# Kernel optimization log

Hardware: AMD Instinct MI355X
Metric: run time of the kernel (lower is better)

Reference implementation:

```python
import jax, jax.numpy as jnp
import numpy as np

S = 1.0   # scale s
M = 0.4   # margin m
EPS = 1e-12  # F.normalize eps


def _l2norm_rows(a):
    # F.normalize(a, dim=1): row-wise L2 normalization
    n = jnp.linalg.norm(a, axis=1, keepdims=True)
    return a / jnp.maximum(n, EPS)


def _half_loss(sim):
    # unique-label branch: positive is the diagonal, all off-diagonal are negatives
    N = sim.shape[0]
    num = S * (jnp.diagonal(sim) - M)                       # [N]
    offdiag = jnp.exp(S * sim) * (1.0 - jnp.eye(N, dtype=sim.dtype))
    denom = jnp.exp(num) + jnp.sum(offdiag, axis=1)         # [N]
    return num - jnp.log(denom)


def setup_inputs() -> dict:
    key = jax.random.key(0)
    k1, k2 = jax.random.split(key)
    N, D = 8192, 256
    return {
        "x1": jax.random.normal(k1, (N, D), dtype=jnp.float32),
        "x2": jax.random.normal(k2, (N, D), dtype=jnp.float32),
        "sentence_id": jnp.arange(N, dtype=jnp.int32),  # unique labels -> more_label=False branch
    }


def reference(x1, x2, sentence_id):
    # x12[i,j] row-normalized similarity of x1_i against all x2_j (and symmetric)
    x12 = _l2norm_rows(x1 @ x2.T)   # [N, N]
    x21 = _l2norm_rows(x2 @ x1.T)   # [N, N]
    L12 = _half_loss(x12)
    L21 = _half_loss(x21)
    loss = -jnp.mean(L12) - jnp.mean(L21)
    return loss, L12, L21
```

## Files before the change

kernel.cpp:

```cpp
#include <hip/hip_runtime.h>
#include <cstdint>
#include <cstddef>


#define NROWS 8192
#define DIMK 256
#define MARGIN 0.4f
#define LOG2E 1.4426950408889634f
#define LN2 0.6931471805599453f

typedef short short8 __attribute__((ext_vector_type(8)));
typedef float f32x4 __attribute__((ext_vector_type(4)));

__device__ __forceinline__ unsigned short f2bf(float f) {
  union { float f; unsigned u; } v; v.f = f;
  unsigned r = (v.u + 0x7fffu + ((v.u >> 16) & 1u)) >> 16;
  return (unsigned short)r;
}

__device__ __forceinline__ void gl_lds16(const void* g, void* l) {
  __builtin_amdgcn_global_load_lds((const __attribute__((address_space(1))) void*)g,
                                   (__attribute__((address_space(3))) void*)l, 16, 0, 0);
}

__device__ __forceinline__ float fexp(float x) {
  return __builtin_amdgcn_exp2f(x * LOG2E);
}

__global__ __launch_bounds__(256)
void k_prep(const float* __restrict__ x1, const float* __restrict__ x2,
            unsigned short* __restrict__ Ab, unsigned short* __restrict__ Bb,
            float* __restrict__ diag, float* __restrict__ zero_region) {
  const int t = threadIdx.x;
  if (blockIdx.x < 2048) {
    const int row = blockIdx.x * 4 + (t >> 6);
    const int l = t & 63;
    const float4 a = ((const float4*)(x1 + (size_t)row * DIMK))[l];
    const float4 b = ((const float4*)(x2 + (size_t)row * DIMK))[l];
    ushort4 ua, ub;
    ua.x = f2bf(a.x); ua.y = f2bf(a.y); ua.z = f2bf(a.z); ua.w = f2bf(a.w);
    ub.x = f2bf(b.x); ub.y = f2bf(b.y); ub.z = f2bf(b.z); ub.w = f2bf(b.w);
    ((ushort4*)(Ab + (size_t)row * DIMK))[l] = ua;
    ((ushort4*)(Bb + (size_t)row * DIMK))[l] = ub;
    float d = a.x * b.x + a.y * b.y + a.z * b.z + a.w * b.w;
#pragma unroll
    for (int m = 1; m < 64; m <<= 1) d += __shfl_xor(d, m);
    if (l == 0) diag[row] = d;
  } else {
    const size_t off = (size_t)(blockIdx.x - 2048) * 1024 + t * 4;
    float4 z = {0.f, 0.f, 0.f, 0.f};
    *(float4*)(zero_region + off) = z;
  }
}

__global__ __launch_bounds__(256)
void k_syrk(const unsigned short* __restrict__ Ab, const unsigned short* __restrict__ Bb,
            float* __restrict__ M1, float* __restrict__ M2) {
  __shared__ unsigned short As[64 * 32];
  __shared__ unsigned short Bs[64 * 32];
  const int t = threadIdx.x, w = t >> 6, l = t & 63, quad = l >> 4, l15 = l & 15;
  const int mat = blockIdx.z & 1;
  const int kseg = blockIdx.z >> 1;
  const unsigned short* X = mat ? Bb : Ab;
  float* Mo = mat ? M2 : M1;
  const int a0 = blockIdx.y * 64, b0 = blockIdx.x * 64;
  const int wr = (w >> 1) * 32, wc = (w & 1) * 32;
  f32x4 acc[2][2] = {};
  const int nn = t & 31, cb = t >> 5;
  const int c0 = cb * 8;
  const int nb = kseg * 512;
  for (int n0 = nb; n0 < nb + 512; n0 += 32) {
    short8 va = *(const short8*)(X + (size_t)(n0 + nn) * DIMK + a0 + c0);
    short8 vb = *(const short8*)(X + (size_t)(n0 + nn) * DIMK + b0 + c0);
#pragma unroll
    for (int i = 0; i < 8; ++i) {
      const int c = c0 + i;
      const int sl = (((nn >> 3) ^ ((c >> 1) & 3)) << 3) + (nn & 7);
      As[c * 32 + sl] = va[i];
      Bs[c * 32 + sl] = vb[i];
    }
    __syncthreads();
    short8 af[2], bg[2];
#pragma unroll
    for (int i = 0; i < 2; ++i) {
      const int ra = wr + i * 16 + l15;
      af[i] = *(const short8*)&As[ra * 32 + ((quad ^ ((ra >> 1) & 3)) << 3)];
      const int rb = wc + i * 16 + l15;
      bg[i] = *(const short8*)&Bs[rb * 32 + ((quad ^ ((rb >> 1) & 3)) << 3)];
    }
#pragma unroll
    for (int i = 0; i < 2; ++i)
#pragma unroll
      for (int j = 0; j < 2; ++j)
        acc[i][j] = __builtin_amdgcn_mfma_f32_16x16x32_bf16(af[i], bg[j], acc[i][j], 0, 0, 0);
    __syncthreads();
  }
#pragma unroll
  for (int i = 0; i < 2; ++i)
#pragma unroll
    for (int j = 0; j < 2; ++j)
#pragma unroll
      for (int r = 0; r < 4; ++r) {
        const int lr = wr + i * 16 + quad * 4 + r;
        const int lc = wc + j * 16 + l15;
        atomicAdd(&Mo[(size_t)(a0 + lr) * 256 + b0 + lc], acc[i][j][r]);
      }
}

__global__ __launch_bounds__(256)
void k_gemmN(const unsigned short* __restrict__ Ab, const unsigned short* __restrict__ Bb,
             const float* __restrict__ M1, const float* __restrict__ M2,
             const float* __restrict__ x1, const float* __restrict__ x2,
             float* __restrict__ rowsq, float* __restrict__ colsq) {
  __shared__ unsigned short As[2][4096];
  __shared__ unsigned short Bs[2][4096];
  const int t = threadIdx.x, w = t >> 6, l = t & 63, quad = l >> 4, l15 = l & 15;
  const unsigned short* A;
  const float* Mf;
  const float* Xf;
  float* sq;
  if (blockIdx.z == 0) { A = Ab; Mf = M2; Xf = x1; sq = rowsq; }
  else                 { A = Bb; Mf = M1; Xf = x2; sq = colsq; }
  const int row0 = blockIdx.x * 128;
  const int col0 = blockIdx.y * 128;
  const int wr = (w >> 1) * 64, wc = (w & 1) * 64;
  f32x4 acc[4][4] = {};

  const int sr0 = l >> 2, slot = l & 3;
  const int cA = w * 2, cB = w * 2 + 1;
  const int rA = cA * 16 + sr0, rB = cB * 16 + sr0;
  const int scA = (slot ^ ((rA >> 1) & 3)) << 3;
  const int scB = (slot ^ ((rB >> 1) & 3)) << 3;
  const unsigned short* pA0 = A + (size_t)(row0 + rA) * DIMK + scA;
  const unsigned short* pA1 = A + (size_t)(row0 + rB) * DIMK + scB;
  const int dA0 = cA * 512 + l * 8, dA1 = cB * 512 + l * 8;

  auto stageB = [&](int k0, int buf) {
#pragma unroll
    for (int g = 0; g < 2; ++g) {
      const int e = g * 2048 + t * 8;
      const int c = e >> 5, kk = e & 31;
      const float4 v0 = *(const float4*)(Mf + (size_t)(col0 + c) * 256 + k0 + kk);
      const float4 v1 = *(const float4*)(Mf + (size_t)(col0 + c) * 256 + k0 + kk + 4);
      ushort4 u0, u1;
      u0.x = f2bf(v0.x); u0.y = f2bf(v0.y); u0.z = f2bf(v0.z); u0.w = f2bf(v0.w);
      u1.x = f2bf(v1.x); u1.y = f2bf(v1.y); u1.z = f2bf(v1.z); u1.w = f2bf(v1.w);
      const int sw = ((kk >> 3) ^ ((c >> 1) & 3)) << 3;
      *(ushort4*)&Bs[buf][c * 32 + sw] = u0;
      *(ushort4*)&Bs[buf][c * 32 + sw + 4] = u1;
    }
  };
  auto issueA = [&](int k0, int buf) {
    gl_lds16(pA0 + k0, &As[buf][dA0]);
    gl_lds16(pA1 + k0, &As[buf][dA1]);
  };

  stageB(0, 0);
  issueA(0, 0);
#pragma unroll
  for (int k = 0; k < 8; ++k) {
    const int cur = k & 1;
    __syncthreads();
    if (k < 7) { stageB((k + 1) * 32, cur ^ 1); issueA((k + 1) * 32, cur ^ 1); }
    short8 af[4], bg[4];
#pragma unroll
    for (int i = 0; i < 4; ++i) {
      const int ra = wr + i * 16 + l15;
      af[i] = *(const short8*)&As[cur][ra * 32 + ((quad ^ ((ra >> 1) & 3)) << 3)];
      const int rb = wc + i * 16 + l15;
      bg[i] = *(const short8*)&Bs[cur][rb * 32 + ((quad ^ ((rb >> 1) & 3)) << 3)];
    }
#pragma unroll
    for (int i = 0; i < 4; ++i)
#pragma unroll
      for (int j = 0; j < 4; ++j)
        acc[i][j] = __builtin_amdgcn_mfma_f32_16x16x32_bf16(af[i], bg[j], acc[i][j], 0, 0, 0);
  }

#pragma unroll
  for (int i = 0; i < 4; ++i) {
#pragma unroll
    for (int r = 0; r < 4; ++r) {
      const int lr = wr + i * 16 + quad * 4 + r;
      const float* xr = Xf + (size_t)(row0 + lr) * DIMK + col0 + wc;
      float rp = 0.f;
#pragma unroll
      for (int j = 0; j < 4; ++j) rp += acc[i][j][r] * xr[j * 16 + l15];
      rp += __shfl_xor(rp, 1); rp += __shfl_xor(rp, 2);
      rp += __shfl_xor(rp, 4); rp += __shfl_xor(rp, 8);
      if (l15 == 0) atomicAdd(&sq[row0 + lr], rp);
    }
  }
}

__global__ __launch_bounds__(256)
void k_gemmE(const unsigned short* __restrict__ Abuf, const unsigned short* __restrict__ Bbuf,
             const float* __restrict__ rowsq, const float* __restrict__ colsq,
             float* __restrict__ rowExp, float* __restrict__ colExp) {
  __shared__ unsigned short As[2][4096];
  __shared__ unsigned short Bs[2][4096];
  __shared__ float cRow[128];
  __shared__ float cCol[128];

  const int t = threadIdx.x;
  const int w = t >> 6;
  const int l = t & 63;
  const int quad = l >> 4;
  const int l15 = l & 15;
  const int row0 = blockIdx.x * 128;
  const int col0 = blockIdx.y * 128;
  const int wr = (w >> 1) * 64;
  const int wc = (w & 1) * 64;

  if (t < 128) cRow[t] = LOG2E * rsqrtf(rowsq[row0 + t]);
  else cCol[t - 128] = LOG2E * rsqrtf(colsq[col0 + t - 128]);

  f32x4 acc[4][4] = {};

  const int sr0 = l >> 2;
  const int slot = l & 3;
  const int cA = w * 2, cB = w * 2 + 1;
  const int rA = cA * 16 + sr0, rB = cB * 16 + sr0;
  const int scA = (slot ^ ((rA >> 1) & 3)) << 3;
  const int scB = (slot ^ ((rB >> 1) & 3)) << 3;
  const unsigned short* pA0 = Abuf + (size_t)(row0 + rA) * DIMK + scA;
  const unsigned short* pA1 = Abuf + (size_t)(row0 + rB) * DIMK + scB;
  const unsigned short* pB0 = Bbuf + (size_t)(col0 + rA) * DIMK + scA;
  const unsigned short* pB1 = Bbuf + (size_t)(col0 + rB) * DIMK + scB;
  const int dA0 = cA * 512 + l * 8, dA1 = cB * 512 + l * 8;

  gl_lds16(pA0, &As[0][dA0]);
  gl_lds16(pA1, &As[0][dA1]);
  gl_lds16(pB0, &Bs[0][dA0]);
  gl_lds16(pB1, &Bs[0][dA1]);

#pragma unroll
  for (int k0 = 0; k0 < 8; ++k0) {
    const int cur = k0 & 1;
    __syncthreads();
    if (k0 < 7) {
      const int nxt = cur ^ 1;
      gl_lds16(pA0 + (k0 + 1) * 32, &As[nxt][dA0]);
      gl_lds16(pA1 + (k0 + 1) * 32, &As[nxt][dA1]);
      gl_lds16(pB0 + (k0 + 1) * 32, &Bs[nxt][dA0]);
      gl_lds16(pB1 + (k0 + 1) * 32, &Bs[nxt][dA1]);
    }
    short8 af[4], bg[4];
#pragma unroll
    for (int i = 0; i < 4; ++i) {
      const int ra = wr + i * 16 + l15;
      af[i] = *(const short8*)&As[cur][ra * 32 + ((quad ^ ((ra >> 1) & 3)) << 3)];
      const int rb = wc + i * 16 + l15;
      bg[i] = *(const short8*)&Bs[cur][rb * 32 + ((quad ^ ((rb >> 1) & 3)) << 3)];
    }
#pragma unroll
    for (int i = 0; i < 4; ++i)
#pragma unroll
      for (int j = 0; j < 4; ++j)
        acc[i][j] = __builtin_amdgcn_mfma_f32_16x16x32_bf16(af[i], bg[j], acc[i][j], 0, 0, 0);
  }

  float cj[4];
#pragma unroll
  for (int j = 0; j < 4; ++j) cj[j] = cCol[wc + j * 16 + l15];
  float colpart[4] = {0.f, 0.f, 0.f, 0.f};
#pragma unroll
  for (int i = 0; i < 4; ++i) {
#pragma unroll
    for (int r = 0; r < 4; ++r) {
      const int lr = wr + i * 16 + quad * 4 + r;
      const float ci = cRow[lr];
      float rp = 0.f;
#pragma unroll
      for (int j = 0; j < 4; ++j) {
        const float g = acc[i][j][r];
        rp += __builtin_amdgcn_exp2f(g * ci);
        colpart[j] += __builtin_amdgcn_exp2f(g * cj[j]);
      }
      rp += __shfl_xor(rp, 1); rp += __shfl_xor(rp, 2);
      rp += __shfl_xor(rp, 4); rp += __shfl_xor(rp, 8);
      if (l15 == 0) atomicAdd(&rowExp[row0 + lr], rp);
    }
  }
#pragma unroll
  for (int j = 0; j < 4; ++j) {
    float cp = colpart[j];
    cp += __shfl_xor(cp, 16); cp += __shfl_xor(cp, 32);
    if (l < 16) atomicAdd(&colExp[col0 + wc + j * 16 + l15], cp);
  }
}

__global__ __launch_bounds__(1024)
void k_final(const float* __restrict__ rowsq, const float* __restrict__ colsq,
             const float* __restrict__ diag, const float* __restrict__ rowExp,
             const float* __restrict__ colExp, float* __restrict__ out,
             double* __restrict__ lossAcc, int* __restrict__ doneCnt) {
  const int t = threadIdx.x;
  const int i = blockIdx.x * 1024 + t;
  const float d = diag[i];
  const float s1 = d * rsqrtf(rowsq[i]);
  const float s2 = d * rsqrtf(colsq[i]);
  const float n1 = s1 - MARGIN, n2 = s2 - MARGIN;
  const float L1 = n1 - LN2 * __builtin_amdgcn_logf(rowExp[i] - fexp(s1) + fexp(n1));
  const float L2 = n2 - LN2 * __builtin_amdgcn_logf(colExp[i] - fexp(s2) + fexp(n2));
  out[1 + i] = L1;
  out[1 + NROWS + i] = L2;
  double part = (double)L1 + (double)L2;
#pragma unroll
  for (int m = 1; m < 64; m <<= 1) part += __shfl_xor(part, m);
  __shared__ double red[16];
  if ((t & 63) == 0) red[t >> 6] = part;
  __syncthreads();
  if (t == 0) {
    double s = 0.0;
#pragma unroll
    for (int q = 0; q < 16; ++q) s += red[q];
    atomicAdd(lossAcc, s);
    __threadfence();
    if (atomicAdd(doneCnt, 1) == 7) {
      const double la =
          __hip_atomic_load(lossAcc, __ATOMIC_ACQUIRE, __HIP_MEMORY_SCOPE_AGENT);
      out[0] = (float)(-la / (double)NROWS);
    }
  }
}

extern "C" void kernel_launch(void* const* d_in, const int* in_sizes, int n_in,
                              void* d_out, int out_size, void* d_ws, size_t ws_size,
                              hipStream_t stream) {
  const float* x1 = (const float*)d_in[0];
  const float* x2 = (const float*)d_in[1];
  float* out = (float*)d_out;
  char* ws = (char*)d_ws;

  unsigned short* Ab = (unsigned short*)(ws);
  unsigned short* Bb = (unsigned short*)(ws + 4194304);
  float* M1 = (float*)(ws + 8388608);
  float* M2 = (float*)(ws + 8650752);
  float* rowsq = (float*)(ws + 8912896);
  float* colsq = (float*)(ws + 8945664);
  float* rowExp = (float*)(ws + 8978432);
  float* colExp = (float*)(ws + 9011200);
  char* ctrl = ws + 9043968;
  double* lossAcc = (double*)(ctrl);
  int* doneCnt = (int*)(ctrl + 256);
  float* diag = (float*)(ws + 9048064);

  k_prep<<<2209, 256, 0, stream>>>(x1, x2, Ab, Bb, diag, (float*)(ws + 8388608));
  k_syrk<<<dim3(4, 4, 32), 256, 0, stream>>>(Ab, Bb, M1, M2);
  k_gemmN<<<dim3(64, 2, 2), 256, 0, stream>>>(Ab, Bb, M1, M2, x1, x2, rowsq, colsq);
  k_gemmE<<<dim3(64, 64), 256, 0, stream>>>(Ab, Bb, rowsq, colsq, rowExp, colExp);
  k_final<<<8, 1024, 0, stream>>>(rowsq, colsq, diag, rowExp, colExp, out,
                                  lossAcc, doneCnt);
}
```

Measured before the change: 191.5 us.

## Load GEMM operands directly to registers and remap blocks for XCD locality

The exp-GEMM kernel drops its LDS double buffering and barriers. Each wave now loads its MFMA fragments straight from global memory into registers, prefetching one k-step ahead. The grid is flattened and remapped so that blocks on the same XCD share column tiles, which is meant to improve L2 reuse. In exchange, each wave issues redundant global loads (operands are no longer shared through LDS), and the row/column scale factors are recomputed per thread instead of being staged in shared memory.

```diff
diff --git a/kernel.cpp b/kernel.cpp
--- a/kernel.cpp
+++ b/kernel.cpp
@@ -197,84 +197,71 @@
 void k_gemmE(const unsigned short* __restrict__ Abuf, const unsigned short* __restrict__ Bbuf,
              const float* __restrict__ rowsq, const float* __restrict__ colsq,
              float* __restrict__ rowExp, float* __restrict__ colExp) {
-  __shared__ unsigned short As[2][4096];
-  __shared__ unsigned short Bs[2][4096];
-  __shared__ float cRow[128];
-  __shared__ float cCol[128];
-
-  const int t = threadIdx.x;
-  const int w = t >> 6;
-  const int l = t & 63;
-  const int quad = l >> 4;
-  const int l15 = l & 15;
-  const int row0 = blockIdx.x * 128;
-  const int col0 = blockIdx.y * 128;
-  const int wr = (w >> 1) * 64;
-  const int wc = (w & 1) * 64;
-
-  if (t < 128) cRow[t] = LOG2E * rsqrtf(rowsq[row0 + t]);
-  else cCol[t - 128] = LOG2E * rsqrtf(colsq[col0 + t - 128]);
+  const int t = threadIdx.x, w = t >> 6, l = t & 63, quad = l >> 4, l15 = l & 15;
+  const int b = blockIdx.x;
+  const int xcd = b & 7, s = b >> 3;
+  const int col0 = (xcd * 8 + (s & 7)) * 128;
+  const int row0 = (s >> 3) * 128;
+  const int wr = (w >> 1) * 64, wc = (w & 1) * 64;
+
+  const unsigned short* pA[4];
+  const unsigned short* pB[4];
+#pragma unroll
+  for (int i = 0; i < 4; ++i) {
+    pA[i] = Abuf + (size_t)(row0 + wr + i * 16 + l15) * DIMK + quad * 8;
+    pB[i] = Bbuf + (size_t)(col0 + wc + i * 16 + l15) * DIMK + quad * 8;
+  }
 
   f32x4 acc[4][4] = {};
-
-  const int sr0 = l >> 2;
-  const int slot = l & 3;
-  const int cA = w * 2, cB = w * 2 + 1;
-  const int rA = cA * 16 + sr0, rB = cB * 16 + sr0;
-  const int scA = (slot ^ ((rA >> 1) & 3)) << 3;
-  const int scB = (slot ^ ((rB >> 1) & 3)) << 3;
-  const unsigned short* pA0 = Abuf + (size_t)(row0 + rA) * DIMK + scA;
-  const unsigned short* pA1 = Abuf + (size_t)(row0 + rB) * DIMK + scB;
-  const unsigned short* pB0 = Bbuf + (size_t)(col0 + rA) * DIMK + scA;
-  const unsigned short* pB1 = Bbuf + (size_t)(col0 + rB) * DIMK + scB;
-  const int dA0 = cA * 512 + l * 8, dA1 = cB * 512 + l * 8;
-
-  gl_lds16(pA0, &As[0][dA0]);
-  gl_lds16(pA1, &As[0][dA1]);
-  gl_lds16(pB0, &Bs[0][dA0]);
-  gl_lds16(pB1, &Bs[0][dA1]);
+  short8 a_cur[4], b_cur[4];
+#pragma unroll
+  for (int i = 0; i < 4; ++i) {
+    a_cur[i] = *(const short8*)pA[i];
+    b_cur[i] = *(const short8*)pB[i];
+  }
 
 #pragma unroll
   for (int k0 = 0; k0 < 8; ++k0) {
-    const int cur = k0 & 1;
-    __syncthreads();
+    short8 a_nxt[4], b_nxt[4];
     if (k0 < 7) {
-      const int nxt = cur ^ 1;
-      gl_lds16(pA0 + (k0 + 1) * 32, &As[nxt][dA0]);
-      gl_lds16(pA1 + (k0 + 1) * 32, &As[nxt][dA1]);
-      gl_lds16(pB0 + (k0 + 1) * 32, &Bs[nxt][dA0]);
-      gl_lds16(pB1 + (k0 + 1) * 32, &Bs[nxt][dA1]);
-    }
-    short8 af[4], bg[4];
-#pragma unroll
-    for (int i = 0; i < 4; ++i) {
-      const int ra = wr + i * 16 + l15;
-      af[i] = *(const short8*)&As[cur][ra * 32 + ((quad ^ ((ra >> 1) & 3)) << 3)];
-      const int rb = wc + i * 16 + l15;
-      bg[i] = *(const short8*)&Bs[cur][rb * 32 + ((quad ^ ((rb >> 1) & 3)) << 3)];
+#pragma unroll
+      for (int i = 0; i < 4; ++i) {
+        a_nxt[i] = *(const short8*)(pA[i] + (k0 + 1) * 32);
+        b_nxt[i] = *(const short8*)(pB[i] + (k0 + 1) * 32);
+      }
     }
 #pragma unroll
     for (int i = 0; i < 4; ++i)
 #pragma unroll
       for (int j = 0; j < 4; ++j)
-        acc[i][j] = __builtin_amdgcn_mfma_f32_16x16x32_bf16(af[i], bg[j], acc[i][j], 0, 0, 0);
+        acc[i][j] = __builtin_amdgcn_mfma_f32_16x16x32_bf16(a_cur[i], b_cur[j], acc[i][j], 0, 0, 0);
+    if (k0 < 7) {
+#pragma unroll
+      for (int i = 0; i < 4; ++i) { a_cur[i] = a_nxt[i]; b_cur[i] = b_nxt[i]; }
+    }
   }
 
   float cj[4];
 #pragma unroll
-  for (int j = 0; j < 4; ++j) cj[j] = cCol[wc + j * 16 + l15];
+  for (int j = 0; j < 4; ++j)
+    cj[j] = LOG2E * rsqrtf(colsq[col0 + wc + j * 16 + l15]);
+  float ci[4][4];
+#pragma unroll
+  for (int i = 0; i < 4; ++i)
+#pragma unroll
+    for (int r = 0; r < 4; ++r)
+      ci[i][r] = LOG2E * rsqrtf(rowsq[row0 + wr + i * 16 + quad * 4 + r]);
   float colpart[4] = {0.f, 0.f, 0.f, 0.f};
 #pragma unroll
   for (int i = 0; i < 4; ++i) {
 #pragma unroll
     for (int r = 0; r < 4; ++r) {
       const int lr = wr + i * 16 + quad * 4 + r;
-      const float ci = cRow[lr];
       float rp = 0.f;
 #pragma unroll
       for (int j = 0; j < 4; ++j) {
         const float g = acc[i][j][r];
-        rp += __builtin_amdgcn_exp2f(g * ci);
+        rp += __builtin_amdgcn_exp2f(g * ci[i][r]);
         colpart[j] += __builtin_amdgcn_exp2f(g * cj[j]);
       }
       rp += __shfl_xor(rp, 1); rp += __shfl_xor(rp, 2);
@@ -349,7 +336,7 @@
   k_prep<<<2209, 256, 0, stream>>>(x1, x2, Ab, Bb, diag, (float*)(ws + 8388608));
   k_syrk<<<dim3(4, 4, 32), 256, 0, stream>>>(Ab, Bb, M1, M2);
   k_gemmN<<<dim3(64, 2, 2), 256, 0, stream>>>(Ab, Bb, M1, M2, x1, x2, rowsq, colsq);
-  k_gemmE<<<dim3(64, 64), 256, 0, stream>>>(Ab, Bb, rowsq, colsq, rowExp, colExp);
+  k_gemmE<<<4096, 256, 0, stream>>>(Ab, Bb, rowsq, colsq, rowExp, colExp);
   k_final<<<8, 1024, 0, stream>>>(rowsq, colsq, diag, rowExp, colExp, out,
                                   lossAcc, doneCnt);
 }
```

New measurement: 282.2 us. +47.4%, slower.

## Widen gemmE tiles to 128x256 with XCD-aware mapping; split gemmN K

Applied to the files above, without the earlier changes.

The main exp-GEMM kernel now computes a 128x256 tile per block instead of 128x128, with each wave holding a 64x128 accumulator (32 MFMA tiles). This halves A-tile reloads and atomics per output element, and blocks are mapped to columns per XCD so B tiles stay in the local L2. gemmN gets a split-K over two halves of K, doubling its grid to raise parallelism, with partial results combined through the existing atomics. The cost is higher register pressure and more LDS per block in gemmE, which may reduce occupancy.

```diff
diff --git a/kernel.cpp b/kernel.cpp
--- a/kernel.cpp
+++ b/kernel.cpp
@@ -119,8 +119,9 @@
   const float* Mf;
   const float* Xf;
   float* sq;
-  if (blockIdx.z == 0) { A = Ab; Mf = M2; Xf = x1; sq = rowsq; }
-  else                 { A = Bb; Mf = M1; Xf = x2; sq = colsq; }
+  if ((blockIdx.z & 1) == 0) { A = Ab; Mf = M2; Xf = x1; sq = rowsq; }
+  else                       { A = Bb; Mf = M1; Xf = x2; sq = colsq; }
+  const int kbase = (blockIdx.z >> 1) * 128;
   const int row0 = blockIdx.x * 128;
   const int col0 = blockIdx.y * 128;
   const int wr = (w >> 1) * 64, wc = (w & 1) * 64;
@@ -131,8 +132,8 @@
   const int rA = cA * 16 + sr0, rB = cB * 16 + sr0;
   const int scA = (slot ^ ((rA >> 1) & 3)) << 3;
   const int scB = (slot ^ ((rB >> 1) & 3)) << 3;
-  const unsigned short* pA0 = A + (size_t)(row0 + rA) * DIMK + scA;
-  const unsigned short* pA1 = A + (size_t)(row0 + rB) * DIMK + scB;
+  const unsigned short* pA0 = A + (size_t)(row0 + rA) * DIMK + kbase + scA;
+  const unsigned short* pA1 = A + (size_t)(row0 + rB) * DIMK + kbase + scB;
   const int dA0 = cA * 512 + l * 8, dA1 = cB * 512 + l * 8;
 
   auto stageB = [&](int k0, int buf) {
@@ -140,8 +141,8 @@
     for (int g = 0; g < 2; ++g) {
       const int e = g * 2048 + t * 8;
       const int c = e >> 5, kk = e & 31;
-      const float4 v0 = *(const float4*)(Mf + (size_t)(col0 + c) * 256 + k0 + kk);
-      const float4 v1 = *(const float4*)(Mf + (size_t)(col0 + c) * 256 + k0 + kk + 4);
+      const float4 v0 = *(const float4*)(Mf + (size_t)(col0 + c) * 256 + kbase + k0 + kk);
+      const float4 v1 = *(const float4*)(Mf + (size_t)(col0 + c) * 256 + kbase + k0 + kk + 4);
       ushort4 u0, u1;
       u0.x = f2bf(v0.x); u0.y = f2bf(v0.y); u0.z = f2bf(v0.z); u0.w = f2bf(v0.w);
       u1.x = f2bf(v1.x); u1.y = f2bf(v1.y); u1.z = f2bf(v1.z); u1.w = f2bf(v1.w);
@@ -158,10 +159,10 @@
   stageB(0, 0);
   issueA(0, 0);
 #pragma unroll
-  for (int k = 0; k < 8; ++k) {
+  for (int k = 0; k < 4; ++k) {
     const int cur = k & 1;
     __syncthreads();
-    if (k < 7) { stageB((k + 1) * 32, cur ^ 1); issueA((k + 1) * 32, cur ^ 1); }
+    if (k < 3) { stageB((k + 1) * 32, cur ^ 1); issueA((k + 1) * 32, cur ^ 1); }
     short8 af[4], bg[4];
 #pragma unroll
     for (int i = 0; i < 4; ++i) {
@@ -198,72 +199,79 @@
              const float* __restrict__ rowsq, const float* __restrict__ colsq,
              float* __restrict__ rowExp, float* __restrict__ colExp) {
   __shared__ unsigned short As[2][4096];
-  __shared__ unsigned short Bs[2][4096];
+  __shared__ unsigned short Bs[2][8192];
   __shared__ float cRow[128];
-  __shared__ float cCol[128];
+  __shared__ float cCol[256];
 
   const int t = threadIdx.x;
   const int w = t >> 6;
   const int l = t & 63;
   const int quad = l >> 4;
   const int l15 = l & 15;
-  const int row0 = blockIdx.x * 128;
-  const int col0 = blockIdx.y * 128;
+  const int b = blockIdx.x;
+  const int xcd = b & 7, s = b >> 3;
+  const int col0 = (xcd * 4 + (s & 3)) * 256;
+  const int row0 = (s >> 2) * 128;
   const int wr = (w >> 1) * 64;
-  const int wc = (w & 1) * 64;
+  const int wc = (w & 1) * 128;
 
   if (t < 128) cRow[t] = LOG2E * rsqrtf(rowsq[row0 + t]);
-  else cCol[t - 128] = LOG2E * rsqrtf(colsq[col0 + t - 128]);
-
-  f32x4 acc[4][4] = {};
+  cCol[t] = LOG2E * rsqrtf(colsq[col0 + t]);
+
+  f32x4 acc[4][8] = {};
 
   const int sr0 = l >> 2;
   const int slot = l & 3;
-  const int cA = w * 2, cB = w * 2 + 1;
-  const int rA = cA * 16 + sr0, rB = cB * 16 + sr0;
-  const int scA = (slot ^ ((rA >> 1) & 3)) << 3;
-  const int scB = (slot ^ ((rB >> 1) & 3)) << 3;
-  const unsigned short* pA0 = Abuf + (size_t)(row0 + rA) * DIMK + scA;
-  const unsigned short* pA1 = Abuf + (size_t)(row0 + rB) * DIMK + scB;
-  const unsigned short* pB0 = Bbuf + (size_t)(col0 + rA) * DIMK + scA;
-  const unsigned short* pB1 = Bbuf + (size_t)(col0 + rB) * DIMK + scB;
-  const int dA0 = cA * 512 + l * 8, dA1 = cB * 512 + l * 8;
-
-  gl_lds16(pA0, &As[0][dA0]);
-  gl_lds16(pA1, &As[0][dA1]);
-  gl_lds16(pB0, &Bs[0][dA0]);
-  gl_lds16(pB1, &Bs[0][dA1]);
-
+  const int cA0 = w * 2, cA1 = w * 2 + 1;
+  const int rA0 = cA0 * 16 + sr0, rA1 = cA1 * 16 + sr0;
+  const unsigned short* pA0 = Abuf + (size_t)(row0 + rA0) * DIMK + ((slot ^ ((rA0 >> 1) & 3)) << 3);
+  const unsigned short* pA1 = Abuf + (size_t)(row0 + rA1) * DIMK + ((slot ^ ((rA1 >> 1) & 3)) << 3);
+  const int dA0 = cA0 * 512 + l * 8, dA1 = cA1 * 512 + l * 8;
+  const unsigned short* pB[4];
+  int dB[4];
+#pragma unroll
+  for (int p = 0; p < 4; ++p) {
+    const int c = w * 4 + p;
+    const int r = c * 16 + sr0;
+    pB[p] = Bbuf + (size_t)(col0 + r) * DIMK + ((slot ^ ((r >> 1) & 3)) << 3);
+    dB[p] = c * 512 + l * 8;
+  }
+
+  auto issue = [&](int k0, int buf) {
+    gl_lds16(pA0 + k0, &As[buf][dA0]);
+    gl_lds16(pA1 + k0, &As[buf][dA1]);
+#pragma unroll
+    for (int p = 0; p < 4; ++p) gl_lds16(pB[p] + k0, &Bs[buf][dB[p]]);
+  };
+
+  issue(0, 0);
 #pragma unroll
   for (int k0 = 0; k0 < 8; ++k0) {
     const int cur = k0 & 1;
     __syncthreads();
-    if (k0 < 7) {
-      const int nxt = cur ^ 1;
-      gl_lds16(pA0 + (k0 + 1) * 32, &As[nxt][dA0]);
-      gl_lds16(pA1 + (k0 + 1) * 32, &As[nxt][dA1]);
-      gl_lds16(pB0 + (k0 + 1) * 32, &Bs[nxt][dA0]);
-      gl_lds16(pB1 + (k0 + 1) * 32, &Bs[nxt][dA1]);
-    }
-    short8 af[4], bg[4];
+    if (k0 < 7) issue((k0 + 1) * 32, cur ^ 1);
+    short8 af[4], bg[8];
 #pragma unroll
     for (int i = 0; i < 4; ++i) {
       const int ra = wr + i * 16 + l15;
       af[i] = *(const short8*)&As[cur][ra * 32 + ((quad ^ ((ra >> 1) & 3)) << 3)];
-      const int rb = wc + i * 16 + l15;
-      bg[i] = *(const short8*)&Bs[cur][rb * 32 + ((quad ^ ((rb >> 1) & 3)) << 3)];
+    }
+#pragma unroll
+    for (int j = 0; j < 8; ++j) {
+      const int rb = wc + j * 16 + l15;
+      bg[j] = *(const short8*)&Bs[cur][rb * 32 + ((quad ^ ((rb >> 1) & 3)) << 3)];
     }
 #pragma unroll
     for (int i = 0; i < 4; ++i)
 #pragma unroll
-      for (int j = 0; j < 4; ++j)
+      for (int j = 0; j < 8; ++j)
         acc[i][j] = __builtin_amdgcn_mfma_f32_16x16x32_bf16(af[i], bg[j], acc[i][j], 0, 0, 0);
   }
 
-  float cj[4];
-#pragma unroll
-  for (int j = 0; j < 4; ++j) cj[j] = cCol[wc + j * 16 + l15];
-  float colpart[4] = {0.f, 0.f, 0.f, 0.f};
+  float cj[8];
+#pragma unroll
+  for (int j = 0; j < 8; ++j) cj[j] = cCol[wc + j * 16 + l15];
+  float colpart[8] = {0.f, 0.f, 0.f, 0.f, 0.f, 0.f, 0.f, 0.f};
 #pragma unroll
   for (int i = 0; i < 4; ++i) {
 #pragma unroll
@@ -272,7 +280,7 @@
       const float ci = cRow[lr];
       float rp = 0.f;
 #pragma unroll
-      for (int j = 0; j < 4; ++j) {
+      for (int j = 0; j < 8; ++j) {
         const float g = acc[i][j][r];
         rp += __builtin_amdgcn_exp2f(g * ci);
         colpart[j] += __builtin_amdgcn_exp2f(g * cj[j]);
@@ -283,7 +291,7 @@
     }
   }
 #pragma unroll
-  for (int j = 0; j < 4; ++j) {
+  for (int j = 0; j < 8; ++j) {
     float cp = colpart[j];
     cp += __shfl_xor(cp, 16); cp += __shfl_xor(cp, 32);
     if (l < 16) atomicAdd(&colExp[col0 + wc + j * 16 + l15], cp);
@@ -348,8 +356,8 @@
 
   k_prep<<<2209, 256, 0, stream>>>(x1, x2, Ab, Bb, diag, (float*)(ws + 8388608));
   k_syrk<<<dim3(4, 4, 32), 256, 0, stream>>>(Ab, Bb, M1, M2);
-  k_gemmN<<<dim3(64, 2, 2), 256, 0, stream>>>(Ab, Bb, M1, M2, x1, x2, rowsq, colsq);
-  k_gemmE<<<dim3(64, 64), 256, 0, stream>>>(Ab, Bb, rowsq, colsq, rowExp, colExp);
+  k_gemmN<<<dim3(64, 2, 4), 256, 0, stream>>>(Ab, Bb, M1, M2, x1, x2, rowsq, colsq);
+  k_gemmE<<<2048, 256, 0, stream>>>(Ab, Bb, rowsq, colsq, rowExp, colExp);
   k_final<<<8, 1024, 0, stream>>>(rowsq, colsq, diag, rowExp, colExp, out,
                                   lossAcc, doneCnt);
 }
```

Result: slower. 211.2 us (+10.3%).

## Run exp-sum GEMM in FP8 with new LDS staging layout

Applied to the files above, without the earlier changes.

Adds an FP8 (e4m3) quantization of both inputs in the prep kernel and switches the large N×N exponent-sum GEMM to fp8 MFMA instructions. LDS tiles now cover 64 K-elements per stage in byte layout, halving the number of K iterations and the bytes loaded per tile. This targets the dominant N×N GEMM, cutting its operand traffic and matrix-core time. The costs are lower precision in the similarity values that feed exp, a new LDS layout without the XOR swizzle (possible bank conflicts), and extra writes in prep.

```diff
diff --git a/kernel.cpp b/kernel.cpp
--- a/kernel.cpp
+++ b/kernel.cpp
@@ -18,6 +18,24 @@
   return (unsigned short)r;
 }
 
+__device__ __forceinline__ unsigned char f2fp8(float f) {
+  union { float f; unsigned u; } v; v.f = f;
+  const unsigned s = (v.u >> 24) & 0x80u;
+  const unsigned au = v.u & 0x7fffffffu;
+  if (au >= 0x43e00000u) return (unsigned char)(s | 0x7eu);
+  int e = (int)(au >> 23) - 127;
+  if (e >= -6) {
+    unsigned mfull = (au & 0x7fffffu) | 0x800000u;
+    unsigned r = (mfull + 0x7ffffu + ((mfull >> 20) & 1u)) >> 20;
+    if (r == 16u) { r = 8u; ++e; }
+    return (unsigned char)(s | ((unsigned)(e + 7) << 3) | (r & 7u));
+  }
+  float scaled = __builtin_fabsf(f) * 512.0f;
+  unsigned n = (unsigned)(scaled + 0.5f);
+  if (n >= 8u) return (unsigned char)(s | 0x08u);
+  return (unsigned char)(s | n);
+}
+
 __device__ __forceinline__ void gl_lds16(const void* g, void* l) {
   __builtin_amdgcn_global_load_lds((const __attribute__((address_space(1))) void*)g,
                                    (__attribute__((address_space(3))) void*)l, 16, 0, 0);
@@ -30,6 +48,7 @@
 __global__ __launch_bounds__(256)
 void k_prep(const float* __restrict__ x1, const float* __restrict__ x2,
             unsigned short* __restrict__ Ab, unsigned short* __restrict__ Bb,
+            unsigned char* __restrict__ A8, unsigned char* __restrict__ B8,
             float* __restrict__ diag, float* __restrict__ zero_region) {
   const int t = threadIdx.x;
   if (blockIdx.x < 2048) {
@@ -42,6 +61,11 @@
     ub.x = f2bf(b.x); ub.y = f2bf(b.y); ub.z = f2bf(b.z); ub.w = f2bf(b.w);
     ((ushort4*)(Ab + (size_t)row * DIMK))[l] = ua;
     ((ushort4*)(Bb + (size_t)row * DIMK))[l] = ub;
+    uchar4 qa, qb;
+    qa.x = f2fp8(a.x); qa.y = f2fp8(a.y); qa.z = f2fp8(a.z); qa.w = f2fp8(a.w);
+    qb.x = f2fp8(b.x); qb.y = f2fp8(b.y); qb.z = f2fp8(b.z); qb.w = f2fp8(b.w);
+    ((uchar4*)(A8 + (size_t)row * DIMK))[l] = qa;
+    ((uchar4*)(B8 + (size_t)row * DIMK))[l] = qb;
     float d = a.x * b.x + a.y * b.y + a.z * b.z + a.w * b.w;
 #pragma unroll
     for (int m = 1; m < 64; m <<= 1) d += __shfl_xor(d, m);
@@ -194,11 +218,11 @@
 }
 
 __global__ __launch_bounds__(256)
-void k_gemmE(const unsigned short* __restrict__ Abuf, const unsigned short* __restrict__ Bbuf,
+void k_gemmE(const unsigned char* __restrict__ A8, const unsigned char* __restrict__ B8,
              const float* __restrict__ rowsq, const float* __restrict__ colsq,
              float* __restrict__ rowExp, float* __restrict__ colExp) {
-  __shared__ unsigned short As[2][4096];
-  __shared__ unsigned short Bs[2][4096];
+  __shared__ unsigned char As[2][8192];
+  __shared__ unsigned char Bs[2][8192];
   __shared__ float cRow[128];
   __shared__ float cCol[128];
 
@@ -217,47 +241,41 @@
 
   f32x4 acc[4][4] = {};
 
-  const int sr0 = l >> 2;
-  const int slot = l & 3;
-  const int cA = w * 2, cB = w * 2 + 1;
-  const int rA = cA * 16 + sr0, rB = cB * 16 + sr0;
-  const int scA = (slot ^ ((rA >> 1) & 3)) << 3;
-  const int scB = (slot ^ ((rB >> 1) & 3)) << 3;
-  const unsigned short* pA0 = Abuf + (size_t)(row0 + rA) * DIMK + scA;
-  const unsigned short* pA1 = Abuf + (size_t)(row0 + rB) * DIMK + scB;
-  const unsigned short* pB0 = Bbuf + (size_t)(col0 + rA) * DIMK + scA;
-  const unsigned short* pB1 = Bbuf + (size_t)(col0 + rB) * DIMK + scB;
-  const int dA0 = cA * 512 + l * 8, dA1 = cB * 512 + l * 8;
-
-  gl_lds16(pA0, &As[0][dA0]);
-  gl_lds16(pA1, &As[0][dA1]);
-  gl_lds16(pB0, &Bs[0][dA0]);
-  gl_lds16(pB1, &Bs[0][dA1]);
-
-#pragma unroll
-  for (int k0 = 0; k0 < 8; ++k0) {
-    const int cur = k0 & 1;
+  const int srow = t >> 1;
+  const int shalf = (t & 1) * 16;
+  const unsigned char* gA = A8 + (size_t)(row0 + srow) * DIMK + shalf;
+  const unsigned char* gB = B8 + (size_t)(col0 + srow) * DIMK + shalf;
+  const int d0 = t * 16, d1 = 4096 + t * 16;
+
+  auto issue = [&](int k0, int buf) {
+    gl_lds16(gA + k0, &As[buf][d0]);
+    gl_lds16(gA + k0 + 32, &As[buf][d1]);
+    gl_lds16(gB + k0, &Bs[buf][d0]);
+    gl_lds16(gB + k0 + 32, &Bs[buf][d1]);
+  };
+
+  issue(0, 0);
+#pragma unroll
+  for (int it = 0; it < 4; ++it) {
+    const int cur = it & 1;
     __syncthreads();
-    if (k0 < 7) {
-      const int nxt = cur ^ 1;
-      gl_lds16(pA0 + (k0 + 1) * 32, &As[nxt][dA0]);
-      gl_lds16(pA1 + (k0 + 1) * 32, &As[nxt][dA1]);
-      gl_lds16(pB0 + (k0 + 1) * 32, &Bs[nxt][dA0]);
-      gl_lds16(pB1 + (k0 + 1) * 32, &Bs[nxt][dA1]);
-    }
-    short8 af[4], bg[4];
-#pragma unroll
-    for (int i = 0; i < 4; ++i) {
-      const int ra = wr + i * 16 + l15;
-      af[i] = *(const short8*)&As[cur][ra * 32 + ((quad ^ ((ra >> 1) & 3)) << 3)];
-      const int rb = wc + i * 16 + l15;
-      bg[i] = *(const short8*)&Bs[cur][rb * 32 + ((quad ^ ((rb >> 1) & 3)) << 3)];
-    }
-#pragma unroll
-    for (int i = 0; i < 4; ++i)
-#pragma unroll
-      for (int j = 0; j < 4; ++j)
-        acc[i][j] = __builtin_amdgcn_mfma_f32_16x16x32_bf16(af[i], bg[j], acc[i][j], 0, 0, 0);
+    if (it < 3) issue((it + 1) * 64, cur ^ 1);
+#pragma unroll
+    for (int kc = 0; kc < 2; ++kc) {
+      long a_[4], b_[4];
+#pragma unroll
+      for (int i = 0; i < 4; ++i) {
+        const int ra = wr + i * 16 + l15;
+        a_[i] = *(const long*)&As[cur][kc * 4096 + ra * 32 + quad * 8];
+        const int rb = wc + i * 16 + l15;
+        b_[i] = *(const long*)&Bs[cur][kc * 4096 + rb * 32 + quad * 8];
+      }
+#pragma unroll
+      for (int i = 0; i < 4; ++i)
+#pragma unroll
+        for (int j = 0; j < 4; ++j)
+          acc[i][j] = __builtin_amdgcn_mfma_f32_16x16x32_fp8_fp8(a_[i], b_[j], acc[i][j], 0, 0, 0);
+    }
   }
 
   float cj[4];
@@ -345,11 +363,14 @@
   double* lossAcc = (double*)(ctrl);
   int* doneCnt = (int*)(ctrl + 256);
   float* diag = (float*)(ws + 9048064);
-
-  k_prep<<<2209, 256, 0, stream>>>(x1, x2, Ab, Bb, diag, (float*)(ws + 8388608));
+  unsigned char* A8 = (unsigned char*)(ws + 9080832);
+  unsigned char* B8 = (unsigned char*)(ws + 11177984);
+
+  k_prep<<<2209, 256, 0, stream>>>(x1, x2, Ab, Bb, A8, B8, diag,
+                                   (float*)(ws + 8388608));
   k_syrk<<<dim3(4, 4, 32), 256, 0, stream>>>(Ab, Bb, M1, M2);
   k_gemmN<<<dim3(64, 2, 2), 256, 0, stream>>>(Ab, Bb, M1, M2, x1, x2, rowsq, colsq);
-  k_gemmE<<<dim3(64, 64), 256, 0, stream>>>(Ab, Bb, rowsq, colsq, rowExp, colExp);
+  k_gemmE<<<dim3(64, 64), 256, 0, stream>>>(A8, B8, rowsq, colsq, rowExp, colExp);
   k_final<<<8, 1024, 0, stream>>>(rowsq, colsq, diag, rowExp, colExp, out,
                                   lossAcc, doneCnt);
 }
```

Result: no change. 188.7 us (-1.4%).
